# Kernel tuning notes

Hardware: AMD Instinct MI355X
Metric: run time of the kernel (lower is better)

## Reference

```python
import jax, jax.numpy as jnp
import numpy as np

N = 20000
E = 320000
IN_DIM = 16
H = 128
HEADS = 4
NEG_SLOPE = 0.2  # GATv2Conv default
EPS_LN = 1e-5


def setup_inputs() -> dict:
    key = jax.random.key(0)
    ks = jax.random.split(key, 16)
    f32 = jnp.float32
    def rn(k, shape, scale):
        return jax.random.normal(k, shape, dtype=f32) * scale
    s_in = 1.0 / np.sqrt(IN_DIM)
    s_h = 1.0 / np.sqrt(H)
    s_4h = 1.0 / np.sqrt(4 * H)
    s_2h = 1.0 / np.sqrt(2 * H)
    inp = {}
    inp["x"] = jax.random.normal(ks[0], (N, IN_DIM), dtype=f32)
    inp["edge_index"] = jax.random.randint(ks[1], (2, E), 0, N)
    inp["edge_attr"] = jax.random.normal(ks[2], (E, 2), dtype=f32)
    inp["emb_w"] = rn(ks[3], (IN_DIM, H), s_in)
    inp["emb_b"] = jnp.zeros((H,), f32)
    # 3 GATv2 layers stacked on leading axis
    inp["lin_l"] = rn(ks[4], (3, H, HEADS * H), s_h)
    inp["lin_r"] = rn(ks[5], (3, H, HEADS * H), s_h)
    inp["lin_edge"] = rn(ks[6], (3, 2, HEADS * H), 1.0 / np.sqrt(2.0))
    inp["att"] = rn(ks[7], (3, HEADS, H), s_h)
    inp["conv_bias01"] = jnp.zeros((2, HEADS * H), f32)  # concat=True layers
    inp["conv_bias2"] = jnp.zeros((H,), f32)             # concat=False layer
    inp["proj_w"] = rn(ks[8], (2, HEADS * H, H), s_4h)
    inp["proj_b"] = jnp.zeros((2, H), f32)
    inp["n1_g"] = jnp.ones((3, H), f32)
    inp["n1_b"] = jnp.zeros((3, H), f32)
    inp["n2_g"] = jnp.ones((3, H), f32)
    inp["n2_b"] = jnp.zeros((3, H), f32)
    inp["ffn_w1"] = rn(ks[9], (3, H, 2 * H), s_h)
    inp["ffn_b1"] = jnp.zeros((3, 2 * H), f32)
    inp["ffn_w2"] = rn(ks[10], (3, 2 * H, H), s_2h)
    inp["ffn_b2"] = jnp.zeros((3, H), f32)
    return inp


def layer_norm(x, g, b):
    mu = jnp.mean(x, axis=-1, keepdims=True)
    var = jnp.mean((x - mu) ** 2, axis=-1, keepdims=True)
    return (x - mu) * jax.lax.rsqrt(var + EPS_LN) * g + b


def gatv2(h, src, dst, eattr, Wl, Wr, We, att, bias, concat, n):
    # h: [n, H]; per-edge gather -> GATv2 attention -> segment softmax -> scatter-add
    xl = (h @ Wl).reshape(n, HEADS, H)   # source transform
    xr = (h @ Wr).reshape(n, HEADS, H)   # target transform
    ee = (eattr @ We).reshape(-1, HEADS, H)
    e = jax.nn.leaky_relu(xl[src] + xr[dst] + ee, NEG_SLOPE)  # [E', HEADS, H]
    score = jnp.einsum('ehc,hc->eh', e, att)                  # [E', HEADS]
    smax = jax.ops.segment_max(score, dst, num_segments=n)
    p = jnp.exp(score - smax[dst])
    denom = jax.ops.segment_sum(p, dst, num_segments=n)
    alpha = p / (denom[dst] + 1e-16)
    out = jax.ops.segment_sum(xl[src] * alpha[..., None], dst, num_segments=n)
    if concat:
        return out.reshape(n, HEADS * H) + bias
    return jnp.mean(out, axis=1) + bias


def reference(x, edge_index, edge_attr, emb_w, emb_b, lin_l, lin_r, lin_edge, att,
              conv_bias01, conv_bias2, proj_w, proj_b, n1_g, n1_b, n2_g, n2_b,
              ffn_w1, ffn_b1, ffn_w2, ffn_b2):
    n = x.shape[0]
    e = edge_attr.shape[0]
    # PyG add_self_loops with fill_value='mean': self-loop attr = mean of incoming edge attrs
    ones = jnp.ones((e,), x.dtype)
    deg = jax.ops.segment_sum(ones, edge_index[1], num_segments=n)
    loop_attr = jax.ops.segment_sum(edge_attr, edge_index[1], num_segments=n) / jnp.maximum(deg, 1.0)[:, None]
    ar = jnp.arange(n)
    src = jnp.concatenate([edge_index[0], ar])
    dst = jnp.concatenate([edge_index[1], ar])
    ea = jnp.concatenate([edge_attr, loop_attr], axis=0)

    h = x @ emb_w + emb_b
    for i in range(3):
        concat = i < 2
        bias = conv_bias01[i] if concat else conv_bias2
        h_in = h
        h = gatv2(h, src, dst, ea, lin_l[i], lin_r[i], lin_edge[i], att[i], bias, concat, n)
        if concat:
            h = h @ proj_w[i] + proj_b[i]
        h = layer_norm(h + h_in, n1_g[i], n1_b[i])
        h2 = h
        h = jax.nn.gelu(h @ ffn_w1[i] + ffn_b1[i], approximate=False) @ ffn_w2[i] + ffn_b2[i]
        h = layer_norm(h + h2, n2_g[i], n2_b[i])
    return h
```

## Files before the change

### kernel.cpp

```cpp
#include <hip/hip_runtime.h>
#include <math.h>

#define IN_DIM 16
#define HDIM   128
#define HEADS  4
#define HH     512
#define FFH    256
#define NEG_SLOPE 0.2f

typedef _Float16 half8 __attribute__((ext_vector_type(8)));
typedef _Float16 h8 __attribute__((ext_vector_type(8)));
typedef _Float16 h4 __attribute__((ext_vector_type(4)));
typedef _Float16 h2 __attribute__((ext_vector_type(2)));
typedef float f32x4 __attribute__((ext_vector_type(4)));
typedef int i32x4 __attribute__((ext_vector_type(4)));

struct __align__(8) Edge { int src; _Float16 ea0, ea1; };

static __device__ inline float hsum8(h8 v) {
    h4 a = __builtin_shufflevector(v, v, 0, 1, 2, 3) +
           __builtin_shufflevector(v, v, 4, 5, 6, 7);
    h2 b = __builtin_shufflevector(a, a, 0, 1) +
           __builtin_shufflevector(a, a, 2, 3);
    return (float)b[0] + (float)b[1];
}

static __device__ inline h8 shfl_xor_h8(h8 v, int off) {
    union { h8 h; i32x4 i; } u;
    u.h = v;
    u.i.x = __shfl_xor(u.i.x, off);
    u.i.y = __shfl_xor(u.i.y, off);
    u.i.z = __shfl_xor(u.i.z, off);
    u.i.w = __shfl_xor(u.i.w, off);
    return u.h;
}

__global__ void xpad_kernel(const float* __restrict__ x, _Float16* __restrict__ xh, int n) {
    int idx = blockIdx.x * 256 + threadIdx.x;
    if (idx >= n * 64) return;
    int r = idx >> 6, k = idx & 63;
    xh[idx] = (k < IN_DIM) ? (_Float16)x[r * IN_DIM + k] : (_Float16)0.0f;
}

struct WDesc { const float* src; _Float16* dst; int Ksrc; int lgKd; int lgN; };
struct WDescs { WDesc d[15]; };
__global__ void wconv_kernel(WDescs ds) {
    WDesc w = ds.d[blockIdx.y];
    int Kd = 1 << w.lgKd;
    int total = 1 << (w.lgKd + w.lgN);
    for (int idx = blockIdx.x * 256 + threadIdx.x; idx < total; idx += gridDim.x * 256) {
        int n2 = idx >> w.lgKd, k = idx & (Kd - 1);
        w.dst[idx] = (k < w.Ksrc) ? (_Float16)w.src[(k << w.lgN) + n2] : (_Float16)0.0f;
    }
}

__global__ void wcvt_kernel(const float* __restrict__ we, const float* __restrict__ att,
                            const float* __restrict__ cb,
                            _Float16* __restrict__ weh, _Float16* __restrict__ atth,
                            _Float16* __restrict__ cbh) {
    int i = blockIdx.x * 256 + threadIdx.x;
    if (i < 3072) weh[i] = (_Float16)we[i];
    else if (i < 4608) atth[i - 3072] = (_Float16)att[i - 3072];
    else if (i < 5632) cbh[i - 4608] = (_Float16)cb[i - 4608];
}

__global__ void deg_kernel(const int* __restrict__ ei, const float* __restrict__ eattr,
                           float* deg, float* asum, int E) {
    int e = blockIdx.x * blockDim.x + threadIdx.x;
    if (e >= E) return;
    int d = ei[E + e];
    atomicAdd(&deg[d], 1.0f);
    atomicAdd(&asum[2 * d], eattr[2 * e]);
    atomicAdd(&asum[2 * d + 1], eattr[2 * e + 1]);
}

__global__ void scan_kernel(const float* __restrict__ deg, int* row_ptr, int* cur, int n) {
    __shared__ int sums[1024];
    int tid = threadIdx.x;
    int per = (n + 1023) / 1024;
    int s0 = tid * per;
    int s1 = s0 + per; if (s1 > n) s1 = n;
    int s = 0;
    for (int i = s0; i < s1; i++) s += (int)deg[i] + 1;
    int mysum = s;
    sums[tid] = s;
    __syncthreads();
    for (int dd = 1; dd < 1024; dd <<= 1) {
        int t = (tid >= dd) ? sums[tid - dd] : 0;
        __syncthreads();
        sums[tid] += t;
        __syncthreads();
    }
    int run = sums[tid] - mysum;
    for (int i = s0; i < s1; i++) {
        row_ptr[i] = run; cur[i] = run;
        run += (int)deg[i] + 1;
    }
    if (tid == 1023) row_ptr[n] = sums[1023];
}

__global__ void scatter_kernel(const int* __restrict__ ei, const float* __restrict__ eattr,
                               const float* __restrict__ deg, const float* __restrict__ asum,
                               int* cur, Edge* csr, int E, int n) {
    int i = blockIdx.x * blockDim.x + threadIdx.x;
    if (i >= E + n) return;
    Edge ed;
    int pos;
    if (i < E) {
        int d = ei[E + i];
        pos = atomicAdd(&cur[d], 1);
        ed.src = ei[i];
        ed.ea0 = (_Float16)eattr[2 * i];
        ed.ea1 = (_Float16)eattr[2 * i + 1];
    } else {
        int nd = i - E;
        float dv = fmaxf(deg[nd], 1.0f);
        pos = atomicAdd(&cur[nd], 1);
        ed.src = nd;
        ed.ea0 = (_Float16)(asum[2 * nd] / dv);
        ed.ea1 = (_Float16)(asum[2 * nd + 1] / dv);
    }
    csr[pos] = ed;
}

template <int KT, int OUTMODE>
__global__ __launch_bounds__(256) void gemm_bstat(const _Float16* __restrict__ A, int lda,
                                                  const _Float16* __restrict__ BT,
                                                  const float* __restrict__ bias,
                                                  float* __restrict__ C32,
                                                  _Float16* __restrict__ C16,
                                                  int M, int Nstride, int numMT) {
    const int PAD = 8, KC = KT / 32;
    __shared__ _Float16 Bs[128][KT + PAD];
    int tid = threadIdx.x;
    int wave = tid >> 6, lane = tid & 63;
    int quad = lane >> 4, l16 = lane & 15;
    int wrow = (wave >> 1) * 32, wcol = (wave & 1) * 64;
    int n0 = blockIdx.x * 128;

#pragma unroll
    for (int t = 0; t < KT / 16; t++) {
        int idx = tid + t * 256;
        int r = idx / (KT / 8), kb = (idx % (KT / 8)) * 8;
        *(half8*)&Bs[r][kb] = *(const half8*)(BT + (size_t)(n0 + r) * KT + kb);
    }
    __syncthreads();

    half8 bfrag[4][KC];
#pragma unroll
    for (int j = 0; j < 4; j++)
#pragma unroll
        for (int kc = 0; kc < KC; kc++)
            bfrag[j][kc] = *(const half8*)&Bs[wcol + j * 16 + l16][kc * 32 + quad * 8];

    float biasj[4];
#pragma unroll
    for (int j = 0; j < 4; j++)
        biasj[j] = bias ? bias[n0 + wcol + j * 16 + l16] : 0.0f;

    for (int mt = blockIdx.y; mt < numMT; mt += gridDim.y) {
        int rbase = mt * 64 + wrow;
        half8 af[2][KC];
#pragma unroll
        for (int i = 0; i < 2; i++) {
            int row = rbase + i * 16 + l16;
#pragma unroll
            for (int kc = 0; kc < KC; kc++)
                af[i][kc] = (row < M) ? *(const half8*)(A + (size_t)row * lda + kc * 32 + quad * 8)
                                      : (half8)(_Float16)0.0f;
        }
        f32x4 acc[2][4] = {};
#pragma unroll
        for (int kc = 0; kc < KC; kc++)
#pragma unroll
            for (int i = 0; i < 2; i++)
#pragma unroll
                for (int j = 0; j < 4; j++)
                    acc[i][j] = __builtin_amdgcn_mfma_f32_16x16x32_f16(af[i][kc], bfrag[j][kc], acc[i][j], 0, 0, 0);
#pragma unroll
        for (int i = 0; i < 2; i++) {
#pragma unroll
            for (int r = 0; r < 4; r++) {
                int row = rbase + i * 16 + quad * 4 + r;
                if (row >= M) continue;
#pragma unroll
                for (int j = 0; j < 4; j++) {
                    int col = n0 + wcol + j * 16 + l16;
                    float v = acc[i][j][r] + biasj[j];
                    if (OUTMODE == 2)
                        C32[(size_t)row * Nstride + col] = v;
                    C16[(size_t)row * Nstride + col] = (_Float16)v;
                }
            }
        }
    }
}

__global__ __launch_bounds__(256) void gemm_ln(const _Float16* __restrict__ A, int lda,
                                               const _Float16* __restrict__ BT,
                                               const float* __restrict__ bias,
                                               const float* __restrict__ R,
                                               const float* __restrict__ g,
                                               const float* __restrict__ b,
                                               float* __restrict__ C32,
                                               _Float16* __restrict__ C16,
                                               int M, int K) {
    const int BK = 64, PAD = 8;
    __shared__ _Float16 As[64][BK + PAD];
    __shared__ _Float16 Bs[128][BK + PAD];
    int tid = threadIdx.x;
    int wave = tid >> 6, lane = tid & 63;
    int quad = lane >> 4, l16 = lane & 15;
    int mBase = blockIdx.x * 64;

    f32x4 acc[8] = {};

    for (int k0 = 0; k0 < K; k0 += BK) {
#pragma unroll
        for (int t = 0; t < 2; t++) {
            int idx = tid + t * 256;
            int r = idx >> 3, kb = (idx & 7) * 8;
            half8 hv = {};
            int grow = mBase + r;
            if (grow < M) hv = *(const half8*)(A + (size_t)grow * lda + k0 + kb);
            *(half8*)&As[r][kb] = hv;
        }
#pragma unroll
        for (int t = 0; t < 4; t++) {
            int idx = tid + t * 256;
            int r = idx >> 3, kb = (idx & 7) * 8;
            *(half8*)&Bs[r][kb] = *(const half8*)(BT + (size_t)r * K + k0 + kb);
        }
        __syncthreads();
#pragma unroll
        for (int kc = 0; kc < 2; kc++) {
            half8 a = *(const half8*)&As[wave * 16 + l16][kc * 32 + quad * 8];
#pragma unroll
            for (int j = 0; j < 8; j++) {
                half8 bb = *(const half8*)&Bs[j * 16 + l16][kc * 32 + quad * 8];
                acc[j] = __builtin_amdgcn_mfma_f32_16x16x32_f16(a, bb, acc[j], 0, 0, 0);
            }
        }
        __syncthreads();
    }

    float gj[8], bj[8], biasj[8];
#pragma unroll
    for (int j = 0; j < 8; j++) {
        int col = j * 16 + l16;
        biasj[j] = bias[col];
        gj[j] = g[col];
        bj[j] = b[col];
    }
    int row0 = mBase + wave * 16 + quad * 4;
    float sum[4] = {}, sq[4] = {};
#pragma unroll
    for (int r = 0; r < 4; r++) {
        int row = row0 + r;
        bool ok = row < M;
        size_t base = (size_t)row * HDIM;
#pragma unroll
        for (int j = 0; j < 8; j++) {
            float v = acc[j][r] + biasj[j] + (ok ? R[base + j * 16 + l16] : 0.0f);
            acc[j][r] = v;
            sum[r] += v;
            sq[r] += v * v;
        }
    }
#pragma unroll
    for (int r = 0; r < 4; r++) {
#pragma unroll
        for (int off = 1; off < 16; off <<= 1) {
            sum[r] += __shfl_xor(sum[r], off);
            sq[r] += __shfl_xor(sq[r], off);
        }
    }
#pragma unroll
    for (int r = 0; r < 4; r++) {
        int row = row0 + r;
        if (row >= M) continue;
        size_t base = (size_t)row * HDIM;
        float mu = sum[r] * (1.0f / HDIM);
        float var = sq[r] * (1.0f / HDIM) - mu * mu;
        float invstd = rsqrtf(var + 1e-5f);
#pragma unroll
        for (int j = 0; j < 8; j++) {
            float o = (acc[j][r] - mu) * invstd * gj[j] + bj[j];
            C32[base + j * 16 + l16] = o;
            if (C16) C16[base + j * 16 + l16] = (_Float16)o;
        }
    }
}

__global__ __launch_bounds__(256) void ffn_fused(const _Float16* __restrict__ A,
                                                 const _Float16* __restrict__ W1T,
                                                 const float* __restrict__ b1,
                                                 const _Float16* __restrict__ W2T,
                                                 const float* __restrict__ b2,
                                                 const float* __restrict__ R,
                                                 const float* __restrict__ g,
                                                 const float* __restrict__ b,
                                                 float* __restrict__ C32,
                                                 _Float16* __restrict__ C16,
                                                 int M) {
    __shared__ _Float16 Ws[128][128 + 8];
    __shared__ _Float16 Mid[64][256 + 8];
    int tid = threadIdx.x;
    int wave = tid >> 6, lane = tid & 63;
    int quad = lane >> 4, l16 = lane & 15;
    int mBase = blockIdx.x * 64;

    half8 afrag[4];
    {
        int row = mBase + wave * 16 + l16;
#pragma unroll
        for (int kc = 0; kc < 4; kc++) {
            if (row < M)
                afrag[kc] = *(const half8*)(A + (size_t)row * HDIM + kc * 32 + quad * 8);
            else
                afrag[kc] = (half8)(_Float16)0.0f;
        }
    }

#pragma unroll
    for (int h = 0; h < 2; h++) {
        if (h) __syncthreads();
#pragma unroll
        for (int t = 0; t < 8; t++) {
            int idx = tid + t * 256;
            int r = idx >> 4, kb = (idx & 15) * 8;
            *(half8*)&Ws[r][kb] = *(const half8*)(W1T + (size_t)(h * 128 + r) * HDIM + kb);
        }
        __syncthreads();
        f32x4 acc[8] = {};
#pragma unroll
        for (int kc = 0; kc < 4; kc++) {
#pragma unroll
            for (int j = 0; j < 8; j++) {
                half8 bb = *(const half8*)&Ws[j * 16 + l16][kc * 32 + quad * 8];
                acc[j] = __builtin_amdgcn_mfma_f32_16x16x32_f16(afrag[kc], bb, acc[j], 0, 0, 0);
            }
        }
#pragma unroll
        for (int j = 0; j < 8; j++) {
            float bj1 = b1[h * 128 + j * 16 + l16];
#pragma unroll
            for (int r = 0; r < 4; r++) {
                float v = acc[j][r] + bj1;
                v = 0.5f * v * (1.0f + erff(v * 0.70710678118654752f));
                Mid[wave * 16 + quad * 4 + r][h * 128 + j * 16 + l16] = (_Float16)v;
            }
        }
    }
    __syncthreads();

    f32x4 acc2[8] = {};
#pragma unroll
    for (int kc2 = 0; kc2 < 2; kc2++) {
        if (kc2) __syncthreads();
#pragma unroll
        for (int t = 0; t < 8; t++) {
            int idx = tid + t * 256;
            int r = idx >> 4, kb = (idx & 15) * 8;
            *(half8*)&Ws[r][kb] = *(const half8*)(W2T + (size_t)r * FFH + kc2 * 128 + kb);
        }
        __syncthreads();
#pragma unroll
        for (int kc = 0; kc < 4; kc++) {
            half8 am = *(const half8*)&Mid[wave * 16 + l16][kc2 * 128 + kc * 32 + quad * 8];
#pragma unroll
            for (int j = 0; j < 8; j++) {
                half8 bb = *(const half8*)&Ws[j * 16 + l16][kc * 32 + quad * 8];
                acc2[j] = __builtin_amdgcn_mfma_f32_16x16x32_f16(am, bb, acc2[j], 0, 0, 0);
            }
        }
    }

    float gj[8], bj[8], b2j[8];
#pragma unroll
    for (int j = 0; j < 8; j++) {
        int col = j * 16 + l16;
        b2j[j] = b2[col];
        gj[j] = g[col];
        bj[j] = b[col];
    }
    int row0 = mBase + wave * 16 + quad * 4;
    float sum[4] = {}, sq[4] = {};
#pragma unroll
    for (int r = 0; r < 4; r++) {
        int row = row0 + r;
        bool ok = row < M;
        size_t base = (size_t)row * HDIM;
#pragma unroll
        for (int j = 0; j < 8; j++) {
            float v = acc2[j][r] + b2j[j] + (ok ? R[base + j * 16 + l16] : 0.0f);
            acc2[j][r] = v;
            sum[r] += v;
            sq[r] += v * v;
        }
    }
#pragma unroll
    for (int r = 0; r < 4; r++) {
#pragma unroll
        for (int off = 1; off < 16; off <<= 1) {
            sum[r] += __shfl_xor(sum[r], off);
            sq[r] += __shfl_xor(sq[r], off);
        }
    }
#pragma unroll
    for (int r = 0; r < 4; r++) {
        int row = row0 + r;
        if (row >= M) continue;
        size_t base = (size_t)row * HDIM;
        float mu = sum[r] * (1.0f / HDIM);
        float var = sq[r] * (1.0f / HDIM) - mu * mu;
        float invstd = rsqrtf(var + 1e-5f);
#pragma unroll
        for (int j = 0; j < 8; j++) {
            float o = (acc2[j][r] - mu) * invstd * gj[j] + bj[j];
            C32[base + j * 16 + l16] = o;
            if (C16) C16[base + j * 16 + l16] = (_Float16)o;
        }
    }
}

__global__ __launch_bounds__(256) void gat_edge_kernel(
    const _Float16* __restrict__ XLR,
    const int* __restrict__ row_ptr, const Edge* __restrict__ csr,
    const _Float16* __restrict__ WEH,
    const _Float16* __restrict__ ATTH,
    const _Float16* __restrict__ CBH,
    const float* __restrict__ cb2,
    _Float16* __restrict__ OUT16, float* __restrict__ OUT32,
    const float* __restrict__ R, const float* __restrict__ lng,
    const float* __restrict__ lnb, _Float16* __restrict__ OUT16h,
    int n, int concat) {
    int tid = threadIdx.x;
    int wave = tid >> 6, lane = tid & 63;
    int g = lane >> 5;
    int sub = lane & 31;
    int node = blockIdx.x * 4 + wave;
    if (node >= n) return;
    int c0 = sub * 16;

    h8 w0[2], w1[2], att[2], xr[2], acc[2];
#pragma unroll
    for (int k = 0; k < 2; k++) {
        w0[k]  = *(const h8*)(WEH + c0 + k * 8);
        w1[k]  = *(const h8*)(WEH + 512 + c0 + k * 8);
        att[k] = *(const h8*)(ATTH + c0 + k * 8);
        acc[k] = (h8)(_Float16)0.0f;
    }
    const _Float16 slope = (_Float16)NEG_SLOPE;

    {
        unsigned nb = ((unsigned)node << 10) + 512u + (unsigned)c0;
        xr[0] = *(const h8*)(XLR + nb);
        xr[1] = *(const h8*)(XLR + nb + 8);
    }

    float m = -1e30f, l = 0.0f;
    int beg = row_ptr[node], end = row_ptr[node + 1];
    int e = beg + g;

    for (; e + 2 < end; e += 4) {
        Edge eg0 = csr[e], eg1 = csr[e + 2];
        unsigned r0 = ((unsigned)eg0.src << 10) + (unsigned)c0;
        unsigned r1 = ((unsigned)eg1.src << 10) + (unsigned)c0;
        h8 x0a = *(const h8*)(XLR + r0);
        h8 x0b = *(const h8*)(XLR + r0 + 8);
        h8 x1a = *(const h8*)(XLR + r1);
        h8 x1b = *(const h8*)(XLR + r1 + 8);

        h8 v;
        h8 p80, p81;
        v = x0a + (xr[0] + w0[0] * eg0.ea0 + w1[0] * eg0.ea1);
        v = __builtin_elementwise_max(v, v * slope);
        p80 = v * att[0];
        v = x0b + (xr[1] + w0[1] * eg0.ea0 + w1[1] * eg0.ea1);
        v = __builtin_elementwise_max(v, v * slope);
        p80 += v * att[1];
        v = x1a + (xr[0] + w0[0] * eg1.ea0 + w1[0] * eg1.ea1);
        v = __builtin_elementwise_max(v, v * slope);
        p81 = v * att[0];
        v = x1b + (xr[1] + w0[1] * eg1.ea0 + w1[1] * eg1.ea1);
        v = __builtin_elementwise_max(v, v * slope);
        p81 += v * att[1];

        float p0 = hsum8(p80);
        float p1 = hsum8(p81);
        p0 += __shfl_xor(p0, 1); p1 += __shfl_xor(p1, 1);
        p0 += __shfl_xor(p0, 2); p1 += __shfl_xor(p1, 2);
        p0 += __shfl_xor(p0, 4); p1 += __shfl_xor(p1, 4);

        float mnew = fmaxf(m, fmaxf(p0, p1));
        float sc  = __expf(m - mnew);
        float e0f = __expf(p0 - mnew);
        float e1f = __expf(p1 - mnew);
        l = l * sc + e0f + e1f;
        _Float16 hs = (_Float16)sc, h0 = (_Float16)e0f, h1 = (_Float16)e1f;
        acc[0] = acc[0] * hs + x0a * h0 + x1a * h1;
        acc[1] = acc[1] * hs + x0b * h0 + x1b * h1;
        m = mnew;
    }
    for (; e < end; e += 2) {
        Edge eg0 = csr[e];
        unsigned r0 = ((unsigned)eg0.src << 10) + (unsigned)c0;
        h8 x0a = *(const h8*)(XLR + r0);
        h8 x0b = *(const h8*)(XLR + r0 + 8);
        h8 v;
        h8 p80;
        v = x0a + (xr[0] + w0[0] * eg0.ea0 + w1[0] * eg0.ea1);
        v = __builtin_elementwise_max(v, v * slope);
        p80 = v * att[0];
        v = x0b + (xr[1] + w0[1] * eg0.ea0 + w1[1] * eg0.ea1);
        v = __builtin_elementwise_max(v, v * slope);
        p80 += v * att[1];
        float p0 = hsum8(p80);
        p0 += __shfl_xor(p0, 1);
        p0 += __shfl_xor(p0, 2);
        p0 += __shfl_xor(p0, 4);
        float mnew = fmaxf(m, p0);
        float sc  = __expf(m - mnew);
        float e0f = __expf(p0 - mnew);
        l = l * sc + e0f;
        _Float16 hs = (_Float16)sc, h0 = (_Float16)e0f;
        acc[0] = acc[0] * hs + x0a * h0;
        acc[1] = acc[1] * hs + x0b * h0;
        m = mnew;
    }

    {
        float m2 = __shfl_xor(m, 32);
        float l2 = __shfl_xor(l, 32);
        h8 a20 = shfl_xor_h8(acc[0], 32);
        h8 a21 = shfl_xor_h8(acc[1], 32);
        float mS = fmaxf(m, m2);
        float sA = __expf(m - mS);
        float sB = __expf(m2 - mS);
        l = l * sA + l2 * sB;
        _Float16 hA = (_Float16)sA, hB = (_Float16)sB;
        acc[0] = acc[0] * hA + a20 * hB;
        acc[1] = acc[1] * hA + a21 * hB;
    }

    float invf = 1.0f / (l + 1e-16f);
    if (concat) {
        _Float16 hi = (_Float16)invf;
        h8 o0 = acc[0] * hi + *(const h8*)(CBH + c0);
        h8 o1 = acc[1] * hi + *(const h8*)(CBH + c0 + 8);
        if (g == 0) {
            unsigned ob = ((unsigned)node << 10) + (unsigned)c0;
            *(h8*)(OUT16 + ob) = o0;
            *(h8*)(OUT16 + ob + 8) = o1;
        }
    } else {
        _Float16 hi = (_Float16)invf;
        h8 t0 = acc[0] * hi;
        h8 t1 = acc[1] * hi;
        t0 = t0 + shfl_xor_h8(t0, 8);
        t1 = t1 + shfl_xor_h8(t1, 8);
        t0 = t0 + shfl_xor_h8(t0, 16);
        t1 = t1 + shfl_xor_h8(t1, 16);
        if (g == 0 && sub < 8) {
            int d0 = sub * 16;
            const float* Rp = R + (size_t)node * HDIM + d0;
            const float* cp = cb2 + d0;
            float v[16];
            float sum = 0.0f, sq = 0.0f;
#pragma unroll
            for (int q = 0; q < 4; q++) {
                f32x4 rv = *(const f32x4*)(Rp + q * 4);
                f32x4 cv = *(const f32x4*)(cp + q * 4);
#pragma unroll
                for (int t = 0; t < 4; t++) {
                    int k2 = q * 4 + t;
                    float base = (k2 < 8) ? (float)t0[k2 & 7] : (float)t1[k2 & 7];
                    float vv = base * 0.25f + cv[t] + rv[t];
                    v[k2] = vv;
                    sum += vv;
                    sq += vv * vv;
                }
            }
            sum += __shfl_xor(sum, 1); sq += __shfl_xor(sq, 1);
            sum += __shfl_xor(sum, 2); sq += __shfl_xor(sq, 2);
            sum += __shfl_xor(sum, 4); sq += __shfl_xor(sq, 4);
            float mu = sum * (1.0f / HDIM);
            float var = sq * (1.0f / HDIM) - mu * mu;
            float invstd = rsqrtf(var + 1e-5f);
            float* op = OUT32 + (size_t)node * HDIM + d0;
            _Float16* oh = OUT16h + (size_t)node * HDIM + d0;
            _Float16 o16[16];
#pragma unroll
            for (int q = 0; q < 4; q++) {
                f32x4 gv = *(const f32x4*)(lng + d0 + q * 4);
                f32x4 bv = *(const f32x4*)(lnb + d0 + q * 4);
                f32x4 ov;
#pragma unroll
                for (int t = 0; t < 4; t++) {
                    float o = (v[q * 4 + t] - mu) * invstd * gv[t] + bv[t];
                    ov[t] = o;
                    o16[q * 4 + t] = (_Float16)o;
                }
                *(f32x4*)(op + q * 4) = ov;
            }
            *(h8*)(oh) = *(h8*)&o16[0];
            *(h8*)(oh + 8) = *(h8*)&o16[8];
        }
    }
}

extern "C" void kernel_launch(void* const* d_in, const int* in_sizes, int n_in,
                              void* d_out, int out_size, void* d_ws, size_t ws_size,
                              hipStream_t stream) {
    const float* x        = (const float*)d_in[0];
    const int*   ei       = (const int*)d_in[1];
    const float* eattr    = (const float*)d_in[2];
    const float* emb_w    = (const float*)d_in[3];
    const float* emb_b    = (const float*)d_in[4];
    const float* lin_l    = (const float*)d_in[5];
    const float* lin_r    = (const float*)d_in[6];
    const float* lin_edge = (const float*)d_in[7];
    const float* attw     = (const float*)d_in[8];
    const float* cb01     = (const float*)d_in[9];
    const float* cb2      = (const float*)d_in[10];
    const float* proj_w   = (const float*)d_in[11];
    const float* proj_b   = (const float*)d_in[12];
    const float* n1g      = (const float*)d_in[13];
    const float* n1b      = (const float*)d_in[14];
    const float* n2g      = (const float*)d_in[15];
    const float* n2b      = (const float*)d_in[16];
    const float* fw1      = (const float*)d_in[17];
    const float* fb1      = (const float*)d_in[18];
    const float* fw2      = (const float*)d_in[19];
    const float* fb2      = (const float*)d_in[20];
    float* out = (float*)d_out;

    const int n = in_sizes[0] / IN_DIM;
    const int E = in_sizes[2] / 2;
    const int EP = E + n;
    const int numMT = (n + 63) / 64;

    size_t off = 0;
    auto alloc = [&](size_t bytes) {
        void* p = (char*)d_ws + off;
        off += (bytes + 255) & ~(size_t)255;
        return p;
    };
    float* deg     = (float*)alloc((size_t)n * 4);
    float* asum    = (float*)alloc((size_t)2 * n * 4);
    int*   row_ptr = (int*)alloc((size_t)(n + 1) * 4);
    int*   cur     = (int*)alloc((size_t)n * 4);
    Edge*  csr     = (Edge*)alloc((size_t)EP * 8);
    float* H0      = (float*)alloc((size_t)n * HDIM * 4);
    float* H1      = (float*)alloc((size_t)n * HDIM * 4);
    _Float16* H0h  = (_Float16*)alloc((size_t)n * HDIM * 2);
    _Float16* H1h  = (_Float16*)alloc((size_t)n * HDIM * 2);
    _Float16* XLR  = (_Float16*)alloc((size_t)n * 1024 * 2);
    _Float16* xh   = (_Float16*)alloc((size_t)n * 64 * 2);
    _Float16* wt_emb  = (_Float16*)alloc((size_t)HDIM * 64 * 2);
    _Float16* wt_llr  = (_Float16*)alloc((size_t)3 * 1024 * HDIM * 2);
    _Float16* wt_proj = (_Float16*)alloc((size_t)2 * HDIM * HH * 2);
    _Float16* wt_f1   = (_Float16*)alloc((size_t)3 * FFH * HDIM * 2);
    _Float16* wt_f2   = (_Float16*)alloc((size_t)3 * HDIM * FFH * 2);
    _Float16* weh     = (_Float16*)alloc((size_t)3 * 1024 * 2);
    _Float16* atth    = (_Float16*)alloc((size_t)3 * 512 * 2);
    _Float16* cbh     = (_Float16*)alloc((size_t)2 * 512 * 2);
    (void)ws_size;

    xpad_kernel<<<(n * 64 + 255) / 256, 256, 0, stream>>>(x, xh, n);
    WDescs ds;
    int di = 0;
    ds.d[di++] = {emb_w, wt_emb, IN_DIM, 6, 7};
    for (int i = 0; i < 3; i++) {
        ds.d[di++] = {lin_l + (size_t)i * HDIM * HH, wt_llr + (size_t)i * 1024 * HDIM, HDIM, 7, 9};
        ds.d[di++] = {lin_r + (size_t)i * HDIM * HH, wt_llr + (size_t)i * 1024 * HDIM + (size_t)512 * HDIM, HDIM, 7, 9};
    }
    for (int i = 0; i < 2; i++)
        ds.d[di++] = {proj_w + (size_t)i * HH * HDIM, wt_proj + (size_t)i * HDIM * HH, HH, 9, 7};
    for (int i = 0; i < 3; i++)
        ds.d[di++] = {fw1 + (size_t)i * HDIM * FFH, wt_f1 + (size_t)i * FFH * HDIM, HDIM, 7, 8};
    for (int i = 0; i < 3; i++)
        ds.d[di++] = {fw2 + (size_t)i * FFH * HDIM, wt_f2 + (size_t)i * HDIM * FFH, FFH, 8, 7};
    wconv_kernel<<<dim3(32, 15), 256, 0, stream>>>(ds);
    wcvt_kernel<<<22, 256, 0, stream>>>(lin_edge, attw, cb01, weh, atth, cbh);

    (void)hipMemsetAsync(deg, 0, (size_t)n * 4, stream);
    (void)hipMemsetAsync(asum, 0, (size_t)2 * n * 4, stream);
    deg_kernel<<<(E + 255) / 256, 256, 0, stream>>>(ei, eattr, deg, asum, E);
    scan_kernel<<<1, 1024, 0, stream>>>(deg, row_ptr, cur, n);
    scatter_kernel<<<(EP + 255) / 256, 256, 0, stream>>>(ei, eattr, deg, asum, cur, csr, E, n);

    gemm_bstat<64, 2><<<dim3(1, numMT), 256, 0, stream>>>(
        xh, 64, wt_emb, emb_b, H0, H0h, n, HDIM, numMT);

    for (int i = 0; i < 3; i++) {
        int concat = (i < 2);
        gemm_bstat<128, 1><<<dim3(8, 80), 256, 0, stream>>>(
            H0h, HDIM, wt_llr + (size_t)i * 1024 * HDIM, nullptr,
            nullptr, XLR, n, 1024, numMT);
        gat_edge_kernel<<<(n + 3) / 4, 256, 0, stream>>>(
            XLR, row_ptr, csr,
            weh + (size_t)i * 1024, atth + (size_t)i * 512,
            concat ? (cbh + (size_t)i * 512) : nullptr, cb2,
            XLR + 512, H1,
            H0, n1g + (size_t)i * HDIM, n1b + (size_t)i * HDIM, H1h,
            n, concat);
        if (concat) {
            gemm_ln<<<(n + 63) / 64, 256, 0, stream>>>(
                XLR + 512, 1024, wt_proj + (size_t)i * HDIM * HH,
                proj_b + (size_t)i * HDIM, H0,
                n1g + (size_t)i * HDIM, n1b + (size_t)i * HDIM,
                H1, H1h, n, HH);
        }
        float* lnout = (i == 2) ? out : H0;
        _Float16* lnout16 = (i == 2) ? nullptr : H0h;
        ffn_fused<<<(n + 63) / 64, 256, 0, stream>>>(
            H1h, wt_f1 + (size_t)i * FFH * HDIM, fb1 + (size_t)i * FFH,
            wt_f2 + (size_t)i * HDIM * FFH, fb2 + (size_t)i * HDIM, H1,
            n2g + (size_t)i * HDIM, n2b + (size_t)i * HDIM,
            lnout, lnout16, n);
    }
}
```

Measured before the change: 564.6 us.

## Split concat-layer GATv2 edge aggregation into two head-half passes

For the two concat layers, the single edge-attention kernel is replaced by two launches of a new kernel. Each launch processes only half of the heads (256 channels per node), using 8 channels per lane and two interleaved edge streams per wave, merged with an online-softmax combine. The goal is to shrink the working set of gathered source rows so it stays better in cache, and to ease register pressure. The cost is an extra launch per layer and re-reading the CSR edge list twice; the last layer keeps the original fused kernel.

After: 586.2 us. +3.8%, slower.

```diff
diff --git a/kernel.cpp b/kernel.cpp
--- a/kernel.cpp
+++ b/kernel.cpp
@@ -421,6 +421,110 @@
             C32[base + j * 16 + l16] = o;
             if (C16) C16[base + j * 16 + l16] = (_Float16)o;
         }
+    }
+}
+
+__global__ __launch_bounds__(256) void gat_half_kernel(
+    const _Float16* __restrict__ XLR,
+    const int* __restrict__ row_ptr, const Edge* __restrict__ csr,
+    const _Float16* __restrict__ WEH,
+    const _Float16* __restrict__ ATTH,
+    const _Float16* __restrict__ CBH,
+    _Float16* __restrict__ OUT16,
+    int n, int half) {
+    int tid = threadIdx.x;
+    int wave = tid >> 6, lane = tid & 63;
+    int g = lane >> 5;
+    int sub = lane & 31;
+    int node = blockIdx.x * 4 + wave;
+    if (node >= n) return;
+    int c0 = half * 256 + sub * 8;
+
+    h8 w0  = *(const h8*)(WEH + c0);
+    h8 w1  = *(const h8*)(WEH + 512 + c0);
+    h8 att = *(const h8*)(ATTH + c0);
+    const _Float16 slope = (_Float16)NEG_SLOPE;
+
+    h8 xr = *(const h8*)(XLR + (((unsigned)node << 10) + 512u + (unsigned)c0));
+    h8 acc = (h8)(_Float16)0.0f;
+    float m = -1e30f, l = 0.0f;
+
+    int beg = row_ptr[node], end = row_ptr[node + 1];
+    int e = beg + g;
+
+    for (; e + 6 < end; e += 8) {
+        Edge eg0 = csr[e], eg1 = csr[e + 2], eg2 = csr[e + 4], eg3 = csr[e + 6];
+        h8 x0 = *(const h8*)(XLR + (((unsigned)eg0.src << 10) + (unsigned)c0));
+        h8 x1 = *(const h8*)(XLR + (((unsigned)eg1.src << 10) + (unsigned)c0));
+        h8 x2 = *(const h8*)(XLR + (((unsigned)eg2.src << 10) + (unsigned)c0));
+        h8 x3 = *(const h8*)(XLR + (((unsigned)eg3.src << 10) + (unsigned)c0));
+
+        h8 v;
+        v = x0 + (xr + w0 * eg0.ea0 + w1 * eg0.ea1);
+        v = __builtin_elementwise_max(v, v * slope);
+        float p0 = hsum8(v * att);
+        v = x1 + (xr + w0 * eg1.ea0 + w1 * eg1.ea1);
+        v = __builtin_elementwise_max(v, v * slope);
+        float p1 = hsum8(v * att);
+        v = x2 + (xr + w0 * eg2.ea0 + w1 * eg2.ea1);
+        v = __builtin_elementwise_max(v, v * slope);
+        float p2 = hsum8(v * att);
+        v = x3 + (xr + w0 * eg3.ea0 + w1 * eg3.ea1);
+        v = __builtin_elementwise_max(v, v * slope);
+        float p3 = hsum8(v * att);
+#pragma unroll
+        for (int off = 1; off < 16; off <<= 1) {
+            p0 += __shfl_xor(p0, off);
+            p1 += __shfl_xor(p1, off);
+            p2 += __shfl_xor(p2, off);
+            p3 += __shfl_xor(p3, off);
+        }
+
+        float mnew = fmaxf(m, fmaxf(fmaxf(p0, p1), fmaxf(p2, p3)));
+        float sc  = __expf(m - mnew);
+        float e0f = __expf(p0 - mnew);
+        float e1f = __expf(p1 - mnew);
+        float e2f = __expf(p2 - mnew);
+        float e3f = __expf(p3 - mnew);
+        l = l * sc + ((e0f + e1f) + (e2f + e3f));
+        acc = acc * (_Float16)sc
+            + (x0 * (_Float16)e0f + x1 * (_Float16)e1f)
+            + (x2 * (_Float16)e2f + x3 * (_Float16)e3f);
+        m = mnew;
+    }
+    for (; e < end; e += 2) {
+        Edge eg0 = csr[e];
+        h8 x0 = *(const h8*)(XLR + (((unsigned)eg0.src << 10) + (unsigned)c0));
+        h8 v = x0 + (xr + w0 * eg0.ea0 + w1 * eg0.ea1);
+        v = __builtin_elementwise_max(v, v * slope);
+        float p0 = hsum8(v * att);
+        p0 += __shfl_xor(p0, 1);
+        p0 += __shfl_xor(p0, 2);
+        p0 += __shfl_xor(p0, 4);
+        p0 += __shfl_xor(p0, 8);
+        float mnew = fmaxf(m, p0);
+        float sc  = __expf(m - mnew);
+        float e0f = __expf(p0 - mnew);
+        l = l * sc + e0f;
+        acc = acc * (_Float16)sc + x0 * (_Float16)e0f;
+        m = mnew;
+    }
+
+    {
+        float m2 = __shfl_xor(m, 32);
+        float l2 = __shfl_xor(l, 32);
+        h8 a2 = shfl_xor_h8(acc, 32);
+        float mS = fmaxf(m, m2);
+        float sA = __expf(m - mS);
+        float sB = __expf(m2 - mS);
+        l = l * sA + l2 * sB;
+        acc = acc * (_Float16)sA + a2 * (_Float16)sB;
+    }
+
+    float invf = 1.0f / (l + 1e-16f);
+    if (g == 0) {
+        h8 o = acc * (_Float16)invf + *(const h8*)(CBH + c0);
+        *(h8*)(OUT16 + (((unsigned)node << 10) + (unsigned)c0)) = o;
     }
 }
 
@@ -699,19 +803,28 @@
         gemm_bstat<128, 1><<<dim3(8, 80), 256, 0, stream>>>(
             H0h, HDIM, wt_llr + (size_t)i * 1024 * HDIM, nullptr,
             nullptr, XLR, n, 1024, numMT);
-        gat_edge_kernel<<<(n + 3) / 4, 256, 0, stream>>>(
-            XLR, row_ptr, csr,
-            weh + (size_t)i * 1024, atth + (size_t)i * 512,
-            concat ? (cbh + (size_t)i * 512) : nullptr, cb2,
-            XLR + 512, H1,
-            H0, n1g + (size_t)i * HDIM, n1b + (size_t)i * HDIM, H1h,
-            n, concat);
         if (concat) {
+            gat_half_kernel<<<(n + 3) / 4, 256, 0, stream>>>(
+                XLR, row_ptr, csr,
+                weh + (size_t)i * 1024, atth + (size_t)i * 512,
+                cbh + (size_t)i * 512, XLR + 512, n, 0);
+            gat_half_kernel<<<(n + 3) / 4, 256, 0, stream>>>(
+                XLR, row_ptr, csr,
+                weh + (size_t)i * 1024, atth + (size_t)i * 512,
+                cbh + (size_t)i * 512, XLR + 512, n, 1);
             gemm_ln<<<(n + 63) / 64, 256, 0, stream>>>(
                 XLR + 512, 1024, wt_proj + (size_t)i * HDIM * HH,
                 proj_b + (size_t)i * HDIM, H0,
                 n1g + (size_t)i * HDIM, n1b + (size_t)i * HDIM,
                 H1, H1h, n, HH);
+        } else {
+            gat_edge_kernel<<<(n + 3) / 4, 256, 0, stream>>>(
+                XLR, row_ptr, csr,
+                weh + (size_t)i * 1024, atth + (size_t)i * 512,
+                nullptr, cb2,
+                XLR + 512, H1,
+                H0, n1g + (size_t)i * HDIM, n1b + (size_t)i * HDIM, H1h,
+                n, concat);
         }
         float* lnout = (i == 2) ? out : H0;
         _Float16* lnout16 = (i == 2) ? nullptr : H0h;
```
